# Performance work log

Measured on AMD Instinct MI355X. Metric: run time of the kernel, lower is better.

The kernel has to match this reference:

```python
import jax, jax.numpy as jnp
import numpy as np

B, S, Q, C = 1, 128, 256, 256
H, DH = 8, 32
TOT = H * DH  # 256


def setup_inputs() -> dict:
    key = jax.random.key(0)
    ks = jax.random.split(key, 12)
    inp = {
        'q_x': jax.random.normal(ks[0], (B, S, Q, C), jnp.float32),
        'kv_x': jax.random.normal(ks[1], (B, S, Q, C), jnp.float32),
        'bias_mask': jax.random.normal(ks[2], (B, S, 1, 1, Q), jnp.float32),
        'bias_pair': jax.random.normal(ks[3], (B, 1, H, Q, Q), jnp.float32),
        # torch nn.Linear weights are (out_features, in_features)
        'Wq': jax.random.normal(ks[4], (TOT, C), jnp.float32) * (C ** -0.5),
        'Wk': jax.random.normal(ks[5], (TOT, C), jnp.float32) * (C ** -0.5),
        'Wv': jax.random.normal(ks[6], (TOT, C), jnp.float32) * (C ** -0.5),
        'Wg': jax.random.normal(ks[7], (TOT, C), jnp.float32) * 0.02,
        'bg': jnp.ones((TOT,), jnp.float32),   # 'gating' init: zero W, bias=1
        'Wo': jax.random.normal(ks[8], (C, TOT), jnp.float32) * 0.02,
        'bo': jnp.zeros((C,), jnp.float32),
    }
    return inp


def reference(q_x, kv_x, bias_mask, bias_pair, Wq, Wk, Wv, Wg, bg, Wo, bo):
    # QKV projections (no bias), split heads, move head dim before Q: [B,S,H,Q,DH]
    def proj(x, W):
        y = jnp.einsum('bsqc,dc->bsqd', x, W)
        return y.reshape(*y.shape[:-1], H, DH).transpose(0, 1, 3, 2, 4)

    q = proj(q_x, Wq)   # NOTE: literal source applies NO 1/sqrt(dh) scaling in naive mode
    k = proj(kv_x, Wk)
    v = proj(kv_x, Wv)

    # scores [B,S,H,Q,K] with additive biases, manual softmax
    scores = jnp.einsum('bshqd,bshkd->bshqk', q, k) + bias_mask + bias_pair
    a = jax.nn.softmax(scores, axis=-1)
    o = jnp.einsum('bshqk,bshkd->bshqd', a, v)
    o = o.transpose(0, 1, 3, 2, 4)  # [B,S,Q,H,DH]

    # gating
    g = jax.nn.sigmoid(jnp.einsum('bsqc,dc->bsqd', q_x, Wg) + bg)
    o = o * g.reshape(*g.shape[:-1], H, DH)

    # output projection
    o = o.reshape(*o.shape[:-2], TOT)
    return jnp.einsum('bsqd,cd->bsqc', o, Wo) + bo
```

## Files before the change

kernel.cpp:

```cpp
#include <hip/hip_runtime.h>


typedef unsigned short u16;
typedef unsigned int   u32;
typedef float  f32x4  __attribute__((ext_vector_type(4)));
typedef __bf16 bf16x8 __attribute__((ext_vector_type(8)));

__device__ __forceinline__ float bf2f(u16 u) {
    union { u32 i; float f; } v; v.i = ((u32)u) << 16; return v.f;
}
__device__ __forceinline__ u16 f2bf(float f) {
    __bf16 h = (__bf16)f; return __builtin_bit_cast(u16, h);
}

__device__ __forceinline__ void gld16(const u16* g, u16* l) {
    __builtin_amdgcn_global_load_lds(
        (const __attribute__((address_space(1))) u32*)g,
        (__attribute__((address_space(3))) u32*)l, 16, 0, 0);
}

__device__ __forceinline__ size_t hm(int row, int col) {
    const int s = row >> 8, q = row & 255, h = col >> 5, dh = col & 31;
    return ((size_t)((h * 128 + s) * 256 + q) << 5) + dh;
}

__device__ __forceinline__ void cvt8(const float4* src, u16* dst) {
    float4 a = src[0], b = src[1];
    u16 r[8];
    r[0] = f2bf(a.x); r[1] = f2bf(a.y); r[2] = f2bf(a.z); r[3] = f2bf(a.w);
    r[4] = f2bf(b.x); r[5] = f2bf(b.y); r[6] = f2bf(b.z); r[7] = f2bf(b.w);
    *(uint4*)dst = *(uint4*)r;
}

__global__ __launch_bounds__(256) void prep(
    const float* __restrict__ qx, const float* __restrict__ kvx,
    const float* __restrict__ Wq, const float* __restrict__ Wk,
    const float* __restrict__ Wv, const float* __restrict__ Wg,
    const float* __restrict__ Wo,
    u16* __restrict__ Xq, u16* __restrict__ Xkv, u16* __restrict__ Wball)
{
    const int b = blockIdx.x, t = threadIdx.x;
    if (b < 4096) {
        const int e = (b * 256 + t) * 8;
        cvt8((const float4*)(qx + e), Xq + e);
    } else if (b < 8192) {
        const int e = ((b - 4096) * 256 + t) * 8;
        cvt8((const float4*)(kvx + e), Xkv + e);
    } else {
        const int b2  = b - 8192;
        const int mat = b2 >> 5;
        const float* W = (mat == 0) ? Wq : (mat == 1) ? Wk : (mat == 2) ? Wv
                       : (mat == 3) ? Wg : Wo;
        const int off = (b2 & 31) * 2048 + t * 8;
        cvt8((const float4*)(W + off), Wball + mat * 65536 + off);
    }
}

__global__ __launch_bounds__(256) void proj_all(
    const u16* __restrict__ Xq, const u16* __restrict__ Xkv,
    const u16* __restrict__ Wball, const float* __restrict__ bg,
    u16* __restrict__ Qh, u16* __restrict__ Kh, u16* __restrict__ Vh, u16* __restrict__ Gh)
{
    __shared__ u16 At[128 * 64];
    __shared__ u16 Wt[128 * 64];

    const int bid = blockIdx.x;
    const int mb  = bid & 255;
    const int nb  = bid >> 8;
    const int t   = nb >> 1;
    const int n0  = (nb & 1) * 128;
    const int m0  = mb * 128;
    const u16* A = (t == 0 || t == 3) ? Xq : Xkv;
    const u16* W = Wball + t * 65536;
    u16*       O = (t == 0) ? Qh : (t == 1) ? Kh : (t == 2) ? Vh : Gh;

    const int tid  = threadIdx.x;
    const int lane = tid & 63;
    const int w    = tid >> 6;
    const int quad = lane >> 4;
    const int ln   = lane & 15;
    const int wm   = (w >> 1) * 64;
    const int wn   = (w & 1) * 64;
    const int lrow = lane >> 3;
    const int lcol = (lane & 7) * 8;

    f32x4 acc[4][4] = {};

    for (int k0 = 0; k0 < 256; k0 += 64) {
        __syncthreads();
        #pragma unroll
        for (int qq = 0; qq < 4; ++qq) {
            const int r = w * 32 + qq * 8;
            gld16(A + (size_t)(m0 + r + lrow) * 256 + k0 + lcol, &At[r * 64]);
            gld16(W + (size_t)(n0 + r + lrow) * 256 + k0 + lcol, &Wt[r * 64]);
        }
        __syncthreads();

        #pragma unroll
        for (int kk = 0; kk < 2; ++kk) {
            const int kc = kk * 32 + quad * 8;
            bf16x8 af[4], bfr[4];
            #pragma unroll
            for (int i = 0; i < 4; ++i)
                af[i] = __builtin_bit_cast(bf16x8, *(const uint4*)&At[(wm + i * 16 + ln) * 64 + kc]);
            #pragma unroll
            for (int j = 0; j < 4; ++j)
                bfr[j] = __builtin_bit_cast(bf16x8, *(const uint4*)&Wt[(wn + j * 16 + ln) * 64 + kc]);
            #pragma unroll
            for (int i = 0; i < 4; ++i)
                #pragma unroll
                for (int j = 0; j < 4; ++j)
                    acc[i][j] = __builtin_amdgcn_mfma_f32_16x16x32_bf16(af[i], bfr[j], acc[i][j], 0, 0, 0);
        }
    }

    const int act = (t == 3);
    #pragma unroll
    for (int i = 0; i < 4; ++i) {
        #pragma unroll
        for (int j = 0; j < 4; ++j) {
            #pragma unroll
            for (int rr = 0; rr < 4; ++rr) {
                const int row = m0 + wm + i * 16 + quad * 4 + rr;
                const int col = n0 + wn + j * 16 + ln;
                float v = acc[i][j][rr];
                if (act) { v += bg[col]; v = 1.0f / (1.0f + __expf(-v)); }
                O[hm(row, col)] = f2bf(v);
            }
        }
    }
}

__global__ __launch_bounds__(256) void gemm_out(
    const u16* __restrict__ Oh, const u16* __restrict__ Wob,
    const float* __restrict__ bo, float* __restrict__ out)
{
    __shared__ u16 At[64 * 64];
    __shared__ u16 Wt[128 * 64];

    const int bid = blockIdx.x;
    const int m0  = (bid & 511) * 64;
    const int n0  = (bid >> 9) * 128;

    const int tid  = threadIdx.x;
    const int lane = tid & 63;
    const int w    = tid >> 6;
    const int quad = lane >> 4;
    const int ln   = lane & 15;
    const int wm   = (w >> 1) * 32;
    const int wn   = (w & 1) * 64;
    const int lrow = lane >> 3;
    const int lcol = (lane & 7) * 8;

    f32x4 acc[2][4] = {};

    for (int k0 = 0; k0 < 256; k0 += 64) {
        __syncthreads();
        #pragma unroll
        for (int qq = 0; qq < 2; ++qq) {
            const int r = w * 16 + qq * 8;
            gld16(Oh + hm(m0 + r + lrow, k0 + lcol), &At[r * 64]);
        }
        #pragma unroll
        for (int qq = 0; qq < 4; ++qq) {
            const int r = w * 32 + qq * 8;
            gld16(Wob + (size_t)(n0 + r + lrow) * 256 + k0 + lcol, &Wt[r * 64]);
        }
        __syncthreads();

        #pragma unroll
        for (int kk = 0; kk < 2; ++kk) {
            const int kc = kk * 32 + quad * 8;
            bf16x8 af[2], bfr[4];
            #pragma unroll
            for (int i = 0; i < 2; ++i)
                af[i] = __builtin_bit_cast(bf16x8, *(const uint4*)&At[(wm + i * 16 + ln) * 64 + kc]);
            #pragma unroll
            for (int j = 0; j < 4; ++j)
                bfr[j] = __builtin_bit_cast(bf16x8, *(const uint4*)&Wt[(wn + j * 16 + ln) * 64 + kc]);
            #pragma unroll
            for (int i = 0; i < 2; ++i)
                #pragma unroll
                for (int j = 0; j < 4; ++j)
                    acc[i][j] = __builtin_amdgcn_mfma_f32_16x16x32_bf16(af[i], bfr[j], acc[i][j], 0, 0, 0);
        }
    }

    #pragma unroll
    for (int i = 0; i < 2; ++i) {
        #pragma unroll
        for (int j = 0; j < 4; ++j) {
            #pragma unroll
            for (int rr = 0; rr < 4; ++rr) {
                const int row = m0 + wm + i * 16 + quad * 4 + rr;
                const int col = n0 + wn + j * 16 + ln;
                out[(size_t)row * 256 + col] = acc[i][j][rr] + bo[col];
            }
        }
    }
}

__global__ __launch_bounds__(256) void attn_kernel(
    const u16* __restrict__ Qh, const u16* __restrict__ Kh, const u16* __restrict__ Vh,
    const u16* __restrict__ Gh, const float* __restrict__ bm, const float* __restrict__ bp,
    u16* __restrict__ Oh)
{
    __shared__ u16   Vt[32][264];
    __shared__ u16   Pl[4][16][268];
    __shared__ float bmf[256];

    const int hs   = blockIdx.x;
    const int h    = hs & 7;
    const int s    = hs >> 3;
    const int qt   = blockIdx.y;
    const int tid  = threadIdx.x;
    const int lane = tid & 63;
    const int w    = tid >> 6;
    const int quad = lane >> 4;
    const int ln   = lane & 15;

    const size_t hsBase = ((size_t)(h * 128 + s) * 256) << 5;

    {
        const uint4* vp = (const uint4*)(Vh + hsBase + (size_t)tid * 32);
        uint4 vv0 = vp[0], vv1 = vp[1], vv2 = vp[2], vv3 = vp[3];
        u16 tmp[32];
        *(uint4*)&tmp[0]  = vv0; *(uint4*)&tmp[8]  = vv1;
        *(uint4*)&tmp[16] = vv2; *(uint4*)&tmp[24] = vv3;
        #pragma unroll
        for (int dh = 0; dh < 32; ++dh) Vt[dh][tid] = tmp[dh];
        bmf[tid] = bm[s * 256 + tid];
    }
    __syncthreads();

    const int q0 = qt * 64 + w * 16;

    bf16x8 aq = __builtin_bit_cast(bf16x8,
        *(const uint4*)(Qh + hsBase + (size_t)(q0 + ln) * 32 + quad * 8));

    f32x4 sc[16];
    #pragma unroll
    for (int nt = 0; nt < 16; ++nt) {
        bf16x8 bk = __builtin_bit_cast(bf16x8,
            *(const uint4*)(Kh + hsBase + (size_t)(nt * 16 + ln) * 32 + quad * 8));
        f32x4 z = {0.f, 0.f, 0.f, 0.f};
        sc[nt] = __builtin_amdgcn_mfma_f32_16x16x32_bf16(aq, bk, z, 0, 0, 0);
    }

    float rmax[4] = {-1e30f, -1e30f, -1e30f, -1e30f};
    #pragma unroll
    for (int nt = 0; nt < 16; ++nt) {
        const int kp = nt * 16 + ln;
        const float bmv = bmf[kp];
        #pragma unroll
        for (int rr = 0; rr < 4; ++rr) {
            const int q = q0 + quad * 4 + rr;
            float v = sc[nt][rr] + bmv + bp[(size_t)(h * 256 + q) * 256 + kp];
            sc[nt][rr] = v;
            rmax[rr] = fmaxf(rmax[rr], v);
        }
    }
    #pragma unroll
    for (int rr = 0; rr < 4; ++rr) {
        float m = rmax[rr];
        m = fmaxf(m, __shfl_xor(m, 1));
        m = fmaxf(m, __shfl_xor(m, 2));
        m = fmaxf(m, __shfl_xor(m, 4));
        m = fmaxf(m, __shfl_xor(m, 8));
        rmax[rr] = m;
    }
    float rsum[4] = {0.f, 0.f, 0.f, 0.f};
    #pragma unroll
    for (int nt = 0; nt < 16; ++nt)
        #pragma unroll
        for (int rr = 0; rr < 4; ++rr) {
            float p = __expf(sc[nt][rr] - rmax[rr]);
            sc[nt][rr] = p;
            rsum[rr] += p;
        }
    float rinv[4];
    #pragma unroll
    for (int rr = 0; rr < 4; ++rr) {
        float t = rsum[rr];
        t += __shfl_xor(t, 1);
        t += __shfl_xor(t, 2);
        t += __shfl_xor(t, 4);
        t += __shfl_xor(t, 8);
        rinv[rr] = 1.0f / t;
    }

    #pragma unroll
    for (int nt = 0; nt < 16; ++nt)
        #pragma unroll
        for (int rr = 0; rr < 4; ++rr)
            Pl[w][quad * 4 + rr][nt * 16 + ln] = f2bf(sc[nt][rr] * rinv[rr]);

    f32x4 o0 = {0.f, 0.f, 0.f, 0.f}, o1 = {0.f, 0.f, 0.f, 0.f};
    #pragma unroll
    for (int kc = 0; kc < 8; ++kc) {
        bf16x8 pa = __builtin_bit_cast(bf16x8, *(const uint4*)&Pl[w][ln][kc * 32 + quad * 8]);
        bf16x8 v0 = __builtin_bit_cast(bf16x8, *(const uint4*)&Vt[ln][kc * 32 + quad * 8]);
        bf16x8 v1 = __builtin_bit_cast(bf16x8, *(const uint4*)&Vt[16 + ln][kc * 32 + quad * 8]);
        o0 = __builtin_amdgcn_mfma_f32_16x16x32_bf16(pa, v0, o0, 0, 0, 0);
        o1 = __builtin_amdgcn_mfma_f32_16x16x32_bf16(pa, v1, o1, 0, 0, 0);
    }

    #pragma unroll
    for (int rr = 0; rr < 4; ++rr) {
        const int q = q0 + quad * 4 + rr;
        const size_t base = hsBase + (size_t)q * 32;
        float g0 = bf2f(Gh[base + ln]);
        float g1 = bf2f(Gh[base + 16 + ln]);
        Oh[base + ln]      = f2bf(o0[rr] * g0);
        Oh[base + 16 + ln] = f2bf(o1[rr] * g1);
    }
}

extern "C" void kernel_launch(void* const* d_in, const int* in_sizes, int n_in,
                              void* d_out, int out_size, void* d_ws, size_t ws_size,
                              hipStream_t stream)
{
    const float* qx  = (const float*)d_in[0];
    const float* kvx = (const float*)d_in[1];
    const float* bm  = (const float*)d_in[2];
    const float* bp  = (const float*)d_in[3];
    const float* Wq  = (const float*)d_in[4];
    const float* Wk  = (const float*)d_in[5];
    const float* Wv  = (const float*)d_in[6];
    const float* Wg  = (const float*)d_in[7];
    const float* bg  = (const float*)d_in[8];
    const float* Wo  = (const float*)d_in[9];
    const float* bo  = (const float*)d_in[10];
    float* out = (float*)d_out;

    const size_t NEL = (size_t)32768 * 256;
    u16* Qh = (u16*)d_ws;
    u16* Kh = Qh + NEL;
    u16* Vh = Kh + NEL;
    u16* Gh = Vh + NEL;
    u16* Wball = Gh + NEL;

    u16* Xq  = (u16*)d_out;
    u16* Xkv = Xq + NEL;

    prep<<<dim3(8352), dim3(256), 0, stream>>>(qx, kvx, Wq, Wk, Wv, Wg, Wo, Xq, Xkv, Wball);

    proj_all<<<dim3(2048), dim3(256), 0, stream>>>(Xq, Xkv, Wball, bg, Qh, Kh, Vh, Gh);

    attn_kernel<<<dim3(1024, 4), dim3(256), 0, stream>>>(Qh, Kh, Vh, Gh, bm, bp, Qh );

    gemm_out<<<dim3(1024), dim3(256), 0, stream>>>(Qh , Wball + 4 * 65536, bo, out);
}
```

Before: 227.3 us.

## Pre-permute pair bias into fragment layout and halve attention grid with reuse

The prep kernel now writes bias_pair into a per-wave, per-fragment float4 layout, so the attention kernel reads it with contiguous vector loads instead of scattered scalar loads. The attention grid is halved: each block handles two query tiles, which reuses the V transpose and mask staging across both. The P tile in LDS shrinks to 64 columns and is processed in four chunks interleaved with the PV MFMAs, and launch bounds now request 5 blocks per SM. The cost is an extra pass over bias_pair in prep, less parallelism in the attention grid, and a smaller, reused P buffer.

```diff
diff --git a/kernel.cpp b/kernel.cpp
--- a/kernel.cpp
+++ b/kernel.cpp
@@ -36,8 +36,9 @@
     const float* __restrict__ qx, const float* __restrict__ kvx,
     const float* __restrict__ Wq, const float* __restrict__ Wk,
     const float* __restrict__ Wv, const float* __restrict__ Wg,
-    const float* __restrict__ Wo,
-    u16* __restrict__ Xq, u16* __restrict__ Xkv, u16* __restrict__ Wball)
+    const float* __restrict__ Wo, const float* __restrict__ bp,
+    u16* __restrict__ Xq, u16* __restrict__ Xkv, u16* __restrict__ Wball,
+    float* __restrict__ bppf)
 {
     const int b = blockIdx.x, t = threadIdx.x;
     if (b < 4096) {
@@ -46,13 +47,30 @@
     } else if (b < 8192) {
         const int e = ((b - 4096) * 256 + t) * 8;
         cvt8((const float4*)(kvx + e), Xkv + e);
-    } else {
+    } else if (b < 8352) {
         const int b2  = b - 8192;
         const int mat = b2 >> 5;
         const float* W = (mat == 0) ? Wq : (mat == 1) ? Wk : (mat == 2) ? Wv
                        : (mat == 3) ? Wg : Wo;
         const int off = (b2 & 31) * 2048 + t * 8;
         cvt8((const float4*)(W + off), Wball + mat * 65536 + off);
+    } else {
+        const int b3 = b - 8352;
+        const int u0 = (b3 * 256 + t) * 2;
+        #pragma unroll
+        for (int k2 = 0; k2 < 2; ++k2) {
+            const int u  = u0 + k2;
+            const int l  = u & 63;
+            const int nt = (u >> 6) & 15;
+            const int tt = u >> 10;
+            const int ww = tt & 3, qqt = (tt >> 2) & 3, hh = tt >> 4;
+            const int qb = qqt * 64 + ww * 16 + (l >> 4) * 4;
+            const int kp = nt * 16 + (l & 15);
+            const float* src = bp + (size_t)(hh * 256 + qb) * 256 + kp;
+            float4 v;
+            v.x = src[0]; v.y = src[256]; v.z = src[512]; v.w = src[768];
+            *(float4*)(bppf + (size_t)u * 4) = v;
+        }
     }
 }
 
@@ -200,19 +218,18 @@
     }
 }
 
-__global__ __launch_bounds__(256) void attn_kernel(
+__global__ __launch_bounds__(256, 5) void attn_kernel(
     const u16* __restrict__ Qh, const u16* __restrict__ Kh, const u16* __restrict__ Vh,
-    const u16* __restrict__ Gh, const float* __restrict__ bm, const float* __restrict__ bp,
+    const u16* __restrict__ Gh, const float* __restrict__ bm, const float* __restrict__ bppf,
     u16* __restrict__ Oh)
 {
     __shared__ u16   Vt[32][264];
-    __shared__ u16   Pl[4][16][268];
+    __shared__ u16   Pl[4][16][76];
     __shared__ float bmf[256];
 
     const int hs   = blockIdx.x;
     const int h    = hs & 7;
     const int s    = hs >> 3;
-    const int qt   = blockIdx.y;
     const int tid  = threadIdx.x;
     const int lane = tid & 63;
     const int w    = tid >> 6;
@@ -233,86 +250,93 @@
     }
     __syncthreads();
 
-    const int q0 = qt * 64 + w * 16;
-
-    bf16x8 aq = __builtin_bit_cast(bf16x8,
-        *(const uint4*)(Qh + hsBase + (size_t)(q0 + ln) * 32 + quad * 8));
-
-    f32x4 sc[16];
-    #pragma unroll
-    for (int nt = 0; nt < 16; ++nt) {
-        bf16x8 bk = __builtin_bit_cast(bf16x8,
-            *(const uint4*)(Kh + hsBase + (size_t)(nt * 16 + ln) * 32 + quad * 8));
-        f32x4 z = {0.f, 0.f, 0.f, 0.f};
-        sc[nt] = __builtin_amdgcn_mfma_f32_16x16x32_bf16(aq, bk, z, 0, 0, 0);
-    }
-
-    float rmax[4] = {-1e30f, -1e30f, -1e30f, -1e30f};
-    #pragma unroll
-    for (int nt = 0; nt < 16; ++nt) {
-        const int kp = nt * 16 + ln;
-        const float bmv = bmf[kp];
+    for (int iq = 0; iq < 2; ++iq) {
+        const int qt = blockIdx.y * 2 + iq;
+        const int q0 = qt * 64 + w * 16;
+
+        bf16x8 aq = __builtin_bit_cast(bf16x8,
+            *(const uint4*)(Qh + hsBase + (size_t)(q0 + ln) * 32 + quad * 8));
+
+        f32x4 sc[16];
+        #pragma unroll
+        for (int nt = 0; nt < 16; ++nt) {
+            bf16x8 bk = __builtin_bit_cast(bf16x8,
+                *(const uint4*)(Kh + hsBase + (size_t)(nt * 16 + ln) * 32 + quad * 8));
+            f32x4 z = {0.f, 0.f, 0.f, 0.f};
+            sc[nt] = __builtin_amdgcn_mfma_f32_16x16x32_bf16(aq, bk, z, 0, 0, 0);
+        }
+
+        const float* bpt = bppf + ((size_t)(((h * 4 + qt) * 4 + w) * 16) * 64 + lane) * 4;
+        float rmax[4] = {-1e30f, -1e30f, -1e30f, -1e30f};
+        #pragma unroll
+        for (int nt = 0; nt < 16; ++nt) {
+            const f32x4 bv = *(const f32x4*)(bpt + (size_t)nt * 256);
+            const float bmv = bmf[nt * 16 + ln];
+            #pragma unroll
+            for (int rr = 0; rr < 4; ++rr) {
+                float v = sc[nt][rr] + bmv + bv[rr];
+                sc[nt][rr] = v;
+                rmax[rr] = fmaxf(rmax[rr], v);
+            }
+        }
+        #pragma unroll
+        for (int rr = 0; rr < 4; ++rr) {
+            float m = rmax[rr];
+            m = fmaxf(m, __shfl_xor(m, 1));
+            m = fmaxf(m, __shfl_xor(m, 2));
+            m = fmaxf(m, __shfl_xor(m, 4));
+            m = fmaxf(m, __shfl_xor(m, 8));
+            rmax[rr] = m;
+        }
+        float rsum[4] = {0.f, 0.f, 0.f, 0.f};
+        #pragma unroll
+        for (int nt = 0; nt < 16; ++nt)
+            #pragma unroll
+            for (int rr = 0; rr < 4; ++rr) {
+                float p = __expf(sc[nt][rr] - rmax[rr]);
+                sc[nt][rr] = p;
+                rsum[rr] += p;
+            }
+        float rinv[4];
+        #pragma unroll
+        for (int rr = 0; rr < 4; ++rr) {
+            float t = rsum[rr];
+            t += __shfl_xor(t, 1);
+            t += __shfl_xor(t, 2);
+            t += __shfl_xor(t, 4);
+            t += __shfl_xor(t, 8);
+            rinv[rr] = 1.0f / t;
+        }
+
+        f32x4 o0 = {0.f, 0.f, 0.f, 0.f}, o1 = {0.f, 0.f, 0.f, 0.f};
+        #pragma unroll
+        for (int c = 0; c < 4; ++c) {
+            #pragma unroll
+            for (int ntl = 0; ntl < 4; ++ntl) {
+                const int nt = c * 4 + ntl;
+                #pragma unroll
+                for (int rr = 0; rr < 4; ++rr)
+                    Pl[w][quad * 4 + rr][ntl * 16 + ln] = f2bf(sc[nt][rr] * rinv[rr]);
+            }
+            #pragma unroll
+            for (int kcl = 0; kcl < 2; ++kcl) {
+                bf16x8 pa = __builtin_bit_cast(bf16x8, *(const uint4*)&Pl[w][ln][kcl * 32 + quad * 8]);
+                bf16x8 v0 = __builtin_bit_cast(bf16x8, *(const uint4*)&Vt[ln][c * 64 + kcl * 32 + quad * 8]);
+                bf16x8 v1 = __builtin_bit_cast(bf16x8, *(const uint4*)&Vt[16 + ln][c * 64 + kcl * 32 + quad * 8]);
+                o0 = __builtin_amdgcn_mfma_f32_16x16x32_bf16(pa, v0, o0, 0, 0, 0);
+                o1 = __builtin_amdgcn_mfma_f32_16x16x32_bf16(pa, v1, o1, 0, 0, 0);
+            }
+        }
+
         #pragma unroll
         for (int rr = 0; rr < 4; ++rr) {
             const int q = q0 + quad * 4 + rr;
-            float v = sc[nt][rr] + bmv + bp[(size_t)(h * 256 + q) * 256 + kp];
-            sc[nt][rr] = v;
-            rmax[rr] = fmaxf(rmax[rr], v);
-        }
-    }
-    #pragma unroll
-    for (int rr = 0; rr < 4; ++rr) {
-        float m = rmax[rr];
-        m = fmaxf(m, __shfl_xor(m, 1));
-        m = fmaxf(m, __shfl_xor(m, 2));
-        m = fmaxf(m, __shfl_xor(m, 4));
-        m = fmaxf(m, __shfl_xor(m, 8));
-        rmax[rr] = m;
-    }
-    float rsum[4] = {0.f, 0.f, 0.f, 0.f};
-    #pragma unroll
-    for (int nt = 0; nt < 16; ++nt)
-        #pragma unroll
-        for (int rr = 0; rr < 4; ++rr) {
-            float p = __expf(sc[nt][rr] - rmax[rr]);
-            sc[nt][rr] = p;
-            rsum[rr] += p;
-        }
-    float rinv[4];
-    #pragma unroll
-    for (int rr = 0; rr < 4; ++rr) {
-        float t = rsum[rr];
-        t += __shfl_xor(t, 1);
-        t += __shfl_xor(t, 2);
-        t += __shfl_xor(t, 4);
-        t += __shfl_xor(t, 8);
-        rinv[rr] = 1.0f / t;
-    }
-
-    #pragma unroll
-    for (int nt = 0; nt < 16; ++nt)
-        #pragma unroll
-        for (int rr = 0; rr < 4; ++rr)
-            Pl[w][quad * 4 + rr][nt * 16 + ln] = f2bf(sc[nt][rr] * rinv[rr]);
-
-    f32x4 o0 = {0.f, 0.f, 0.f, 0.f}, o1 = {0.f, 0.f, 0.f, 0.f};
-    #pragma unroll
-    for (int kc = 0; kc < 8; ++kc) {
-        bf16x8 pa = __builtin_bit_cast(bf16x8, *(const uint4*)&Pl[w][ln][kc * 32 + quad * 8]);
-        bf16x8 v0 = __builtin_bit_cast(bf16x8, *(const uint4*)&Vt[ln][kc * 32 + quad * 8]);
-        bf16x8 v1 = __builtin_bit_cast(bf16x8, *(const uint4*)&Vt[16 + ln][kc * 32 + quad * 8]);
-        o0 = __builtin_amdgcn_mfma_f32_16x16x32_bf16(pa, v0, o0, 0, 0, 0);
-        o1 = __builtin_amdgcn_mfma_f32_16x16x32_bf16(pa, v1, o1, 0, 0, 0);
-    }
-
-    #pragma unroll
-    for (int rr = 0; rr < 4; ++rr) {
-        const int q = q0 + quad * 4 + rr;
-        const size_t base = hsBase + (size_t)q * 32;
-        float g0 = bf2f(Gh[base + ln]);
-        float g1 = bf2f(Gh[base + 16 + ln]);
-        Oh[base + ln]      = f2bf(o0[rr] * g0);
-        Oh[base + 16 + ln] = f2bf(o1[rr] * g1);
+            const size_t base = hsBase + (size_t)q * 32;
+            float g0 = bf2f(Gh[base + ln]);
+            float g1 = bf2f(Gh[base + 16 + ln]);
+            Oh[base + ln]      = f2bf(o0[rr] * g0);
+            Oh[base + 16 + ln] = f2bf(o1[rr] * g1);
+        }
     }
 }
 
@@ -339,15 +363,17 @@
     u16* Vh = Kh + NEL;
     u16* Gh = Vh + NEL;
     u16* Wball = Gh + NEL;
+    float* bppf = (float*)(Wball + 5 * 65536);
 
     u16* Xq  = (u16*)d_out;
     u16* Xkv = Xq + NEL;
 
-    prep<<<dim3(8352), dim3(256), 0, stream>>>(qx, kvx, Wq, Wk, Wv, Wg, Wo, Xq, Xkv, Wball);
+    prep<<<dim3(8608), dim3(256), 0, stream>>>(qx, kvx, Wq, Wk, Wv, Wg, Wo, bp,
+                                               Xq, Xkv, Wball, bppf);
 
     proj_all<<<dim3(2048), dim3(256), 0, stream>>>(Xq, Xkv, Wball, bg, Qh, Kh, Vh, Gh);
 
-    attn_kernel<<<dim3(1024, 4), dim3(256), 0, stream>>>(Qh, Kh, Vh, Gh, bm, bp, Qh );
+    attn_kernel<<<dim3(1024, 2), dim3(256), 0, stream>>>(Qh, Kh, Vh, Gh, bm, bppf, Qh );
 
     gemm_out<<<dim3(1024), dim3(256), 0, stream>>>(Qh , Wball + 4 * 65536, bo, out);
 }
```

Result: slower. 299.9 us (+31.9%).
